# Performance work log

Hardware: AMD Instinct MI355X
Metric: run time of the kernel (lower is better)

The kernel has to match this reference:

```python
import jax, jax.numpy as jnp
import numpy as np

COMMITMENT_COST = 0.25
N_TOKENS = 32768
NUM_EMBEDDINGS = 8192
EMBEDDING_DIM = 256


def setup_inputs() -> dict:
    key = jax.random.key(0)
    k1, k2 = jax.random.split(key)
    z_e = jax.random.normal(k1, (N_TOKENS, EMBEDDING_DIM), dtype=jnp.float32)
    embeddings = jax.random.normal(k2, (NUM_EMBEDDINGS, EMBEDDING_DIM), dtype=jnp.float32)
    return {"z_e": z_e, "embeddings": embeddings}


def reference(z_e, embeddings):
    # Pairwise squared L2 distances: ||z||^2 - 2 z.e + ||e||^2  -> (N, K)
    z_sq = jnp.sum(z_e * z_e, axis=-1, keepdims=True)          # (N, 1)
    e_sq = jnp.sum(embeddings * embeddings, axis=-1)            # (K,)
    cross = jnp.einsum('nd,kd->nk', z_e, embeddings)            # (N, K) GEMM
    distances = z_sq - 2.0 * cross + e_sq[None, :]
    encoding_indices = jnp.argmin(distances, axis=1)            # (N,)
    z_q = embeddings[encoding_indices]                          # gather (N, D)

    sg = jax.lax.stop_gradient
    commitment_loss = jnp.mean((sg(z_e) - z_q) ** 2)
    embedding_loss = jnp.mean((z_e - sg(z_q)) ** 2)
    vq_loss = embedding_loss + COMMITMENT_COST * commitment_loss

    # straight-through estimator
    z_q_st = z_e + sg(z_q - z_e)
    return z_q_st, vq_loss, encoding_indices
```

## Files before the change

### kernel.cpp

```cpp
#include <hip/hip_runtime.h>

typedef float f32x4 __attribute__((ext_vector_type(4)));
typedef short s16x8 __attribute__((ext_vector_type(8)));

#define NT 32768
#define NK 8192
#define ND 256
#define NSP 32
#define NKT 12

static __device__ __forceinline__ ushort f2bf(float f) {
  unsigned u = __float_as_uint(f);
  unsigned r = (u + 0x7FFFu + ((u >> 16) & 1u)) >> 16;
  return (ushort)r;
}

__global__ __launch_bounds__(256) void vq_cvt(const float* __restrict__ src,
                                              ushort* __restrict__ dst) {
  size_t idx = (size_t)blockIdx.x * 256 + threadIdx.x;
  size_t n = idx >> 6;
  int dq = (int)(idx & 63) * 4;
  float4 v = *reinterpret_cast<const float4*>(src + n * ND + dq);
  float f[4] = {v.x, v.y, v.z, v.w};
  ushort h[4], l[4];
#pragma unroll
  for (int t = 0; t < 4; ++t) {
    h[t] = f2bf(f[t]);
    float hf = __uint_as_float((unsigned)h[t] << 16);
    l[t] = f2bf(f[t] - hf);
  }
  *reinterpret_cast<ushort4*>(dst + n * 512 + dq) = make_ushort4(h[0], h[1], h[2], h[3]);
  *reinterpret_cast<ushort4*>(dst + n * 512 + 256 + dq) = make_ushort4(l[0], l[1], l[2], l[3]);
}

__global__ __launch_bounds__(256) void vq_esq(const float* __restrict__ emb,
                                              float* __restrict__ esq) {
  int w = threadIdx.x >> 6, lane = threadIdx.x & 63;
  int k = blockIdx.x * 4 + w;
  const float4 e = *reinterpret_cast<const float4*>(emb + (size_t)k * ND + lane * 4);
  float s = e.x * e.x + e.y * e.y + e.z * e.z + e.w * e.w;
#pragma unroll
  for (int off = 32; off >= 1; off >>= 1) s += __shfl_down(s, off);
  if (lane == 0) esq[k] = s;
}

#define GL16(gp, lp)                                                              \
  __builtin_amdgcn_global_load_lds(                                               \
      (const __attribute__((address_space(1))) unsigned int*)(gp),                \
      (__attribute__((address_space(3))) unsigned int*)(lp), 16, 0, 0)

#define BAR()                                                                     \
  do {                                                                            \
    asm volatile("" ::: "memory");                                                \
    __builtin_amdgcn_s_barrier();                                                 \
    asm volatile("" ::: "memory");                                                \
  } while (0)

__device__ __forceinline__ int koffA(int kt) { return ((kt >= 8) ? 256 : 0) + (kt & 3) * 64; }
__device__ __forceinline__ int koffB(int kt) { return ((kt >= 4 && kt < 8) ? 256 : 0) + (kt & 3) * 64; }

__global__ __launch_bounds__(512, 2) void vq_mfma(
    const ushort* __restrict__ z2, const ushort* __restrict__ e2,
    const float* __restrict__ esq, float* __restrict__ pdist,
    int* __restrict__ pidx) {
  __shared__ __align__(16) char smem[131072];
  char* ldsA = smem;
  char* ldsB = smem + 65536;

  const int gid = blockIdx.x;
  const int x = gid & 7, c = gid >> 3;
  const int S = x * 8 + (c >> 6);
  const int wi = c & 63;
  const int mt = (S >> 2) * 8 + (wi >> 3);
  const int nt = (S & 3) * 8 + (wi & 7);
  const int m0 = mt * 256, n0 = nt * 256;

  const int tid = threadIdx.x, lane = tid & 63, wid = tid >> 6;
  const int wr = wid >> 2, wc = wid & 3;
  const int fr = lane & 15, g = lane >> 4;

  const int sslot = (tid & 3) ^ ((tid >> 3) & 3);
  const ushort* aBase = z2 + (size_t)(m0 + (tid >> 2)) * 512 + sslot * 8;
  const ushort* bBase = e2 + (size_t)(n0 + (tid >> 2)) * 512 + sslot * 8;

#define STAGE_A(kt, kh)                                                           \
  do {                                                                            \
    const ushort* _g = aBase + koffA(kt) + (kh) * 32;                             \
    char* _l = ldsA + (((kt) & 1) << 15) + ((kh) << 14) + tid * 16;               \
    GL16(_g, _l);                                                                 \
    GL16(_g + 65536, _l + 8192);                                                  \
  } while (0)
#define STAGE_B(kt, kh)                                                           \
  do {                                                                            \
    const ushort* _g = bBase + koffB(kt) + (kh) * 32;                             \
    char* _l = ldsB + (((kt) & 1) << 15) + ((kh) << 14) + tid * 16;               \
    GL16(_g, _l);                                                                 \
    GL16(_g + 65536, _l + 8192);                                                  \
  } while (0)

  const int lbyte = fr * 64 + (((g ^ (fr >> 1)) & 3) << 4);
  const int aro = wr * 8192 + lbyte;
  const int bro = wc * 4096 + lbyte;

  f32x4 acc[8][4];
  const f32x4 zero = {0.f, 0.f, 0.f, 0.f};
#pragma unroll
  for (int i = 0; i < 8; ++i)
#pragma unroll
    for (int j = 0; j < 4; ++j) acc[i][j] = zero;

  STAGE_A(0, 0); STAGE_B(0, 0); STAGE_A(0, 1); STAGE_B(0, 1);
  STAGE_A(1, 0); STAGE_B(1, 0); STAGE_A(1, 1);
  asm volatile("s_waitcnt vmcnt(6)" ::: "memory");
  BAR();

#define MMACC(J0, J1)                                                             \
  do {                                                                            \
    __builtin_amdgcn_s_setprio(1);                                                \
    _Pragma("unroll") for (int i = 0; i < 8; ++i) {                               \
      acc[i][J0] = __builtin_amdgcn_mfma_f32_16x16x32_bf16(af[i], b0, acc[i][J0], 0, 0, 0); \
      acc[i][J1] = __builtin_amdgcn_mfma_f32_16x16x32_bf16(af[i], b1, acc[i][J1], 0, 0, 0); \
    }                                                                             \
    __builtin_amdgcn_s_setprio(0);                                                \
  } while (0)

#pragma unroll 2
  for (int kt = 0; kt < NKT; ++kt) {
    const int bufo = (kt & 1) << 15;
    const char* pa = ldsA + bufo + aro;
    const char* pb = ldsB + bufo + bro;
    s16x8 af[8], b0, b1;

    b0 = *(const s16x8*)(pb);
    b1 = *(const s16x8*)(pb + 1024);
#pragma unroll
    for (int i = 0; i < 8; ++i) af[i] = *(const s16x8*)(pa + i * 1024);
    if (kt + 1 < NKT) STAGE_B(kt + 1, 1);
    BAR();
    MMACC(0, 1);
    BAR();

    b0 = *(const s16x8*)(pb + 2048);
    b1 = *(const s16x8*)(pb + 3072);
    if (kt + 2 < NKT) STAGE_A(kt + 2, 0);
    BAR();
    MMACC(2, 3);
    BAR();

    b0 = *(const s16x8*)(pb + 16384);
    b1 = *(const s16x8*)(pb + 16384 + 1024);
#pragma unroll
    for (int i = 0; i < 8; ++i) af[i] = *(const s16x8*)(pa + 16384 + i * 1024);
    if (kt + 2 < NKT) STAGE_B(kt + 2, 0);
    BAR();
    MMACC(0, 1);
    BAR();

    b0 = *(const s16x8*)(pb + 16384 + 2048);
    b1 = *(const s16x8*)(pb + 16384 + 3072);
    if (kt + 2 < NKT) STAGE_A(kt + 2, 1);
    BAR();
    MMACC(2, 3);
    if (kt == NKT - 2) {
      asm volatile("s_waitcnt vmcnt(0)" ::: "memory");
    } else {
      asm volatile("s_waitcnt vmcnt(6)" ::: "memory");
    }
    BAR();
  }

  float eqv[4];
#pragma unroll
  for (int j = 0; j < 4; ++j) eqv[j] = esq[n0 + wc * 64 + j * 16 + fr];

  float* rdv = (float*)smem;
  unsigned char* rdc = (unsigned char*)(smem + 98304);

#pragma unroll
  for (int i = 0; i < 8; ++i)
#pragma unroll
    for (int r = 0; r < 4; ++r) {
      float bv = 3.4e38f; int bc = 0;
#pragma unroll
      for (int j = 0; j < 4; ++j) {
        float dist = fmaf(-2.f, acc[i][j][r], eqv[j]);
        int cl = wc * 64 + j * 16 + fr;
        if (dist < bv) { bv = dist; bc = cl; }
      }
      int row = wr * 128 + i * 16 + g * 4 + r;
      rdv[row * 67 + wc * 16 + fr] = bv;
      rdc[row * 64 + wc * 16 + fr] = (unsigned char)bc;
    }
  BAR();
  {
    const int row = tid >> 1, h = tid & 1;
    const float* pv = rdv + row * 67 + h * 32;
    const unsigned char* pc = rdc + row * 64 + h * 32;
    float bv = 3.4e38f; int bc = 256;
#pragma unroll
    for (int s = 0; s < 32; ++s) {
      float v = pv[s]; int cc = pc[s];
      if (v < bv || (v == bv && cc < bc)) { bv = v; bc = cc; }
    }
    float ov = __shfl_xor(bv, 1);
    int oc = __shfl_xor(bc, 1);
    if (ov < bv || (ov == bv && oc < bc)) { bv = ov; bc = oc; }
    if (h == 0) {
      int n = m0 + row;
      pdist[(size_t)n * NSP + nt] = bv;
      pidx[(size_t)n * NSP + nt] = n0 + bc;
    }
  }
}

__global__ __launch_bounds__(256) void vq_gather(
    const float* __restrict__ z, const float* __restrict__ emb,
    const float* __restrict__ pdist, const int* __restrict__ pidx,
    float* __restrict__ out, float* __restrict__ lpart) {
  int w = threadIdx.x >> 6, lane = threadIdx.x & 63;
  int n = blockIdx.x * 4 + w;
  int p = lane & (NSP - 1);
  float d = pdist[(size_t)n * NSP + p];
  int ii = pidx[(size_t)n * NSP + p];
#pragma unroll
  for (int off = 1; off < NSP; off <<= 1) {
    float od = __shfl_xor(d, off);
    int oi = __shfl_xor(ii, off);
    if (od < d || (od == d && oi < ii)) { d = od; ii = oi; }
  }
  int bi = ii;
  float4 q = *reinterpret_cast<const float4*>(emb + (size_t)bi * ND + lane * 4);
  float4 zz = *reinterpret_cast<const float4*>(z + (size_t)n * ND + lane * 4);
  *reinterpret_cast<float4*>(out + (size_t)n * ND + lane * 4) = q;
  float dx = zz.x - q.x, dy = zz.y - q.y, dz = zz.z - q.z, dw = zz.w - q.w;
  float s2 = dx * dx + dy * dy + dz * dz + dw * dw;
#pragma unroll
  for (int off = 32; off >= 1; off >>= 1) s2 += __shfl_down(s2, off);
  __shared__ float ls[4];
  if (lane == 0) {
    ls[w] = s2;
    out[(size_t)NT * ND + 1 + n] = (float)bi;
  }
  __syncthreads();
  if (threadIdx.x == 0) lpart[blockIdx.x] = ls[0] + ls[1] + ls[2] + ls[3];
}

__global__ __launch_bounds__(256) void vq_finalize(const float* __restrict__ lpart,
                                                   float* __restrict__ out) {
  __shared__ float s[256];
  float acc = 0.f;
  for (int i = threadIdx.x; i < NT / 4; i += 256) acc += lpart[i];
  s[threadIdx.x] = acc;
  __syncthreads();
  for (int st = 128; st >= 1; st >>= 1) {
    if (threadIdx.x < st) s[threadIdx.x] += s[threadIdx.x + st];
    __syncthreads();
  }
  if (threadIdx.x == 0)
    out[(size_t)NT * ND] = 1.25f * s[0] / (float)((size_t)NT * ND);
}

extern "C" void kernel_launch(void* const* d_in, const int* in_sizes, int n_in,
                              void* d_out, int out_size, void* d_ws, size_t ws_size,
                              hipStream_t stream) {
  const float* z = (const float*)d_in[0];
  const float* emb = (const float*)d_in[1];
  float* out = (float*)d_out;

  float* esq = (float*)d_ws;
  ushort* z2 = (ushort*)(esq + NK);
  ushort* e2 = z2 + (size_t)NT * 512;
  float* pdist = (float*)(e2 + (size_t)NK * 512);
  int* pidx = (int*)(pdist + (size_t)NT * NSP);
  float* lpart = (float*)(pidx + (size_t)NT * NSP);

  vq_cvt<<<NT / 4, 256, 0, stream>>>(z, z2);
  vq_cvt<<<NK / 4, 256, 0, stream>>>(emb, e2);
  vq_esq<<<NK / 4, 256, 0, stream>>>(emb, esq);
  vq_mfma<<<4096, 512, 0, stream>>>(z2, e2, esq, pdist, pidx);
  vq_gather<<<NT / 4, 256, 0, stream>>>(z, emb, pdist, pidx, out, lpart);
  vq_finalize<<<1, 256, 0, stream>>>(lpart, out);
}
```

Baseline: 453.7 us.

## Replace multi-barrier staggered pipeline with simple one-barrier-per-tile double buffering

```diff
diff --git a/kernel.cpp b/kernel.cpp
--- a/kernel.cpp
+++ b/kernel.cpp
@@ -110,62 +110,42 @@
     for (int j = 0; j < 4; ++j) acc[i][j] = zero;
 
   STAGE_A(0, 0); STAGE_B(0, 0); STAGE_A(0, 1); STAGE_B(0, 1);
-  STAGE_A(1, 0); STAGE_B(1, 0); STAGE_A(1, 1);
-  asm volatile("s_waitcnt vmcnt(6)" ::: "memory");
+  asm volatile("s_waitcnt vmcnt(0)" ::: "memory");
   BAR();
-
-#define MMACC(J0, J1)                                                             \
-  do {                                                                            \
-    __builtin_amdgcn_s_setprio(1);                                                \
-    _Pragma("unroll") for (int i = 0; i < 8; ++i) {                               \
-      acc[i][J0] = __builtin_amdgcn_mfma_f32_16x16x32_bf16(af[i], b0, acc[i][J0], 0, 0, 0); \
-      acc[i][J1] = __builtin_amdgcn_mfma_f32_16x16x32_bf16(af[i], b1, acc[i][J1], 0, 0, 0); \
-    }                                                                             \
-    __builtin_amdgcn_s_setprio(0);                                                \
-  } while (0)
 
 #pragma unroll 2
   for (int kt = 0; kt < NKT; ++kt) {
     const int bufo = (kt & 1) << 15;
     const char* pa = ldsA + bufo + aro;
     const char* pb = ldsB + bufo + bro;
-    s16x8 af[8], b0, b1;
-
-    b0 = *(const s16x8*)(pb);
-    b1 = *(const s16x8*)(pb + 1024);
+
+    if (kt + 1 < NKT) {
+      STAGE_A(kt + 1, 0); STAGE_B(kt + 1, 0);
+      STAGE_A(kt + 1, 1); STAGE_B(kt + 1, 1);
+    }
+
+    s16x8 af[8], bf[4];
+#pragma unroll
+    for (int j = 0; j < 4; ++j) bf[j] = *(const s16x8*)(pb + j * 1024);
 #pragma unroll
     for (int i = 0; i < 8; ++i) af[i] = *(const s16x8*)(pa + i * 1024);
-    if (kt + 1 < NKT) STAGE_B(kt + 1, 1);
-    BAR();
-    MMACC(0, 1);
-    BAR();
-
-    b0 = *(const s16x8*)(pb + 2048);
-    b1 = *(const s16x8*)(pb + 3072);
-    if (kt + 2 < NKT) STAGE_A(kt + 2, 0);
-    BAR();
-    MMACC(2, 3);
-    BAR();
-
-    b0 = *(const s16x8*)(pb + 16384);
-    b1 = *(const s16x8*)(pb + 16384 + 1024);
+#pragma unroll
+    for (int i = 0; i < 8; ++i)
+#pragma unroll
+      for (int j = 0; j < 4; ++j)
+        acc[i][j] = __builtin_amdgcn_mfma_f32_16x16x32_bf16(af[i], bf[j], acc[i][j], 0, 0, 0);
+#pragma unroll
+    for (int j = 0; j < 4; ++j) bf[j] = *(const s16x8*)(pb + 16384 + j * 1024);
 #pragma unroll
     for (int i = 0; i < 8; ++i) af[i] = *(const s16x8*)(pa + 16384 + i * 1024);
-    if (kt + 2 < NKT) STAGE_B(kt + 2, 0);
-    BAR();
-    MMACC(0, 1);
-    BAR();
-
-    b0 = *(const s16x8*)(pb + 16384 + 2048);
-    b1 = *(const s16x8*)(pb + 16384 + 3072);
-    if (kt + 2 < NKT) STAGE_A(kt + 2, 1);
-    BAR();
-    MMACC(2, 3);
-    if (kt == NKT - 2) {
-      asm volatile("s_waitcnt vmcnt(0)" ::: "memory");
-    } else {
-      asm volatile("s_waitcnt vmcnt(6)" ::: "memory");
-    }
+#pragma unroll
+    for (int i = 0; i < 8; ++i)
+#pragma unroll
+      for (int j = 0; j < 4; ++j)
+        acc[i][j] = __builtin_amdgcn_mfma_f32_16x16x32_bf16(af[i], bf[j], acc[i][j], 0, 0, 0);
+
+    asm volatile("s_waitcnt vmcnt(0) lgkmcnt(0)" ::: "memory");
+    __builtin_amdgcn_sched_barrier(0);
     BAR();
   }
 
```

Result: no change. 447.7 us (-1.3%).
